# Kernel optimization log

Hardware: AMD Instinct MI355X
Metric: run time of the kernel (lower is better)

The kernel has to match this reference:

```python
import jax, jax.numpy as jnp
import numpy as np

B, N_UNITS, SEQ, H = 4, 1024, 2048, 8
D_HEAD = N_UNITS // H
SCALE = 1.0 / D_HEAD ** 0.5


def setup_inputs() -> dict:
    key = jax.random.key(0)
    k1, k2, k3 = jax.random.split(key, 3)
    x = jax.random.normal(k1, (B, N_UNITS, SEQ), dtype=jnp.float32)
    # conv1x1 weights, bias=False; scaled like typical init
    W_qkv = jax.random.normal(k2, (3 * N_UNITS, N_UNITS), dtype=jnp.float32) * (1.0 / N_UNITS ** 0.5)
    W_out = jax.random.normal(k3, (N_UNITS, N_UNITS), dtype=jnp.float32) * (1.0 / N_UNITS ** 0.5)
    return {"x": x, "W_qkv": W_qkv, "W_out": W_out}


def reference(x, W_qkv, W_out):
    # x: (B, n_units, S). Conv1x1 == per-position linear along channel dim.
    qkv = jnp.einsum('oc,bcs->bos', W_qkv, x)          # (B, 3*n_units, S)
    Q, K, V = jnp.split(qkv, 3, axis=1)                # each (B, n_units, S)
    # torch.chunk along channels into h heads == reshape (B, h, d_head, S)
    Q = Q.reshape(B, H, D_HEAD, SEQ)
    K = K.reshape(B, H, D_HEAD, SEQ)
    V = V.reshape(B, H, D_HEAD, SEQ)
    # scores: Q^T K * scale  (NO softmax in original module; mask unused)
    A = jnp.einsum('bhdq,bhdk->bhqk', Q, K) * SCALE    # (B, h, S, S)
    # aggregation: sum_k A[q,k] * V[d,k]  (original does broadcast mul+sum)
    C = jnp.einsum('bhqk,bhdk->bhdq', A, V)            # (B, h, d_head, S)
    C = C.reshape(B, N_UNITS, SEQ)
    out = jnp.einsum('oc,bcs->bos', W_out, C)          # (B, n_units, S)
    return out
```

## Files before the change

### kernel.cpp

```cpp
#include <hip/hip_runtime.h>
#include <hip/hip_bf16.h>
#include <stdint.h>

using bf16 = __hip_bfloat16;

typedef __bf16 bf16x8 __attribute__((ext_vector_type(8)));
typedef float  f32x4  __attribute__((ext_vector_type(4)));

constexpr int Bc = 4, Hh = 8, Dh = 128, S = 2048, Cn = 1024, O3 = 3072;
constexpr float SCALE = 0.08838834764831845f;

#define GLDS16(gp, lp)                                               \
  __builtin_amdgcn_global_load_lds(                                  \
      (const __attribute__((address_space(1))) void*)(gp),           \
      (__attribute__((address_space(3))) void*)(lp), 16, 0, 0)

#define WAITVM(N) asm volatile("s_waitcnt vmcnt(" #N ")" ::: "memory")
#define BAR()                                  \
  do {                                         \
    asm volatile("" ::: "memory");             \
    __builtin_amdgcn_s_barrier();              \
    asm volatile("" ::: "memory");             \
  } while (0)

__device__ __forceinline__ void gemm_bt_core(
    const bf16* __restrict__ Abase, int lda,
    const bf16* __restrict__ Bbase, int ldb,
    int kIters, f32x4 (&acc)[4][4])
{
  alignas(16) __shared__ bf16 As[128 * 32];
  alignas(16) __shared__ bf16 Bs[128 * 32];
  const int t    = threadIdx.x;
  const int lane = t & 63;
  const int quad = lane >> 4, r16 = lane & 15;
  const int wave = t >> 6;
  const int wm = (wave & 1) * 64, wn = (wave >> 1) * 64;
  const int lrow = lane >> 2;
  const int lk   = (lane & 3) * 8;

  const long aOff0 = (long)(wave * 32 + lrow) * lda + lk;
  const long aOff1 = aOff0 + 16l * lda;
  const long bOff0 = (long)(wave * 32 + lrow) * ldb + lk;
  const long bOff1 = bOff0 + 16l * ldb;
  bf16* aL0 = &As[(wave * 32) * 32];
  bf16* aL1 = &As[(wave * 32 + 16) * 32];
  bf16* bL0 = &Bs[(wave * 32) * 32];
  bf16* bL1 = &Bs[(wave * 32 + 16) * 32];

#pragma unroll
  for (int i = 0; i < 4; i++)
#pragma unroll
    for (int j = 0; j < 4; j++) acc[i][j] = {0.f, 0.f, 0.f, 0.f};

  for (int ks = 0; ks < kIters; ++ks) {
    const int k0 = ks * 32;
    __syncthreads();
    GLDS16(Abase + k0 + aOff0, aL0);
    GLDS16(Abase + k0 + aOff1, aL1);
    GLDS16(Bbase + k0 + bOff0, bL0);
    GLDS16(Bbase + k0 + bOff1, bL1);
    __syncthreads();
    bf16x8 af[4], bfr[4];
#pragma unroll
    for (int i = 0; i < 4; i++)
      af[i] = *(const bf16x8*)&As[(wm + i * 16 + r16) * 32 + quad * 8];
#pragma unroll
    for (int j = 0; j < 4; j++)
      bfr[j] = *(const bf16x8*)&Bs[(wn + j * 16 + r16) * 32 + quad * 8];
#pragma unroll
    for (int i = 0; i < 4; i++)
#pragma unroll
      for (int j = 0; j < 4; j++)
        acc[i][j] = __builtin_amdgcn_mfma_f32_16x16x32_bf16(af[i], bfr[j], acc[i][j], 0, 0, 0);
  }
}

__device__ __forceinline__ void store_bf16_tile(
    f32x4 (&acc)[4][4], bf16* __restrict__ Cp, int ldc)
{
  const int t = threadIdx.x;
  const int lane = t & 63;
  const int quad = lane >> 4, r16 = lane & 15;
  const int wave = t >> 6;
  const int wm = (wave & 1) * 64, wn = (wave >> 1) * 64;
#pragma unroll
  for (int i = 0; i < 4; i++)
#pragma unroll
    for (int j = 0; j < 4; j++)
#pragma unroll
      for (int r = 0; r < 4; r++) {
        const int row = wm + i * 16 + quad * 4 + r;
        const int col = wn + j * 16 + r16;
        Cp[(long)row * ldc + col] = __float2bfloat16(acc[i][j][r]);
      }
}

__device__ __forceinline__ void store_f32_tile(
    f32x4 (&acc)[4][4], float* __restrict__ Cp, int ldc)
{
  const int t = threadIdx.x;
  const int lane = t & 63;
  const int quad = lane >> 4, r16 = lane & 15;
  const int wave = t >> 6;
  const int wm = (wave & 1) * 64, wn = (wave >> 1) * 64;
#pragma unroll
  for (int i = 0; i < 4; i++)
#pragma unroll
    for (int j = 0; j < 4; j++)
#pragma unroll
      for (int r = 0; r < 4; r++) {
        const int row = wm + i * 16 + quad * 4 + r;
        const int col = wn + j * 16 + r16;
        Cp[(long)row * ldc + col] = acc[i][j][r];
      }
}

__global__ __launch_bounds__(512, 2) void k_gemm_kv8(
    const bf16* __restrict__ WkvB, const bf16* __restrict__ xT, bf16* __restrict__ KV)
{
  constexpr int NT = Cn / 32;
  alignas(16) __shared__ bf16 smem[4 * 16384];

  const int orig = blockIdx.x;
  const int swz  = (orig & 7) * 32 + (orig >> 3);
  const int mt = swz >> 5;
  const int nt = swz & 31;
  const int m0 = mt * 256;

  const int tid  = threadIdx.x;
  const int lane = tid & 63;
  const int w    = tid >> 6;
  const int quad = lane >> 4, r16 = lane & 15;
  const int wm = (w >> 2) * 128;
  const int wn = (w & 3) * 64;

  const int srow = w * 16 + (lane >> 2);
  const int cx   = (lane & 3) ^ ((lane >> 3) & 3);
  const bf16* Ag = WkvB + (long)(m0 + srow) * Cn + cx * 8;
  const bf16* Bg = xT + (long)((long)nt * 256 + srow) * Cn + cx * 8;
  const int ldsW = w * 512;

#define KV8_STAGE_A(tt)                                                   \
  do {                                                                    \
    const int k0_ = (tt) * 32, bb_ = ((tt) & 3) * 16384;                  \
    GLDS16(Ag + k0_,            &smem[bb_ + ldsW]);                       \
    GLDS16(Ag + 128l * Cn + k0_, &smem[bb_ + 4096 + ldsW]);               \
  } while (0)
#define KV8_STAGE_B(tt)                                                   \
  do {                                                                    \
    const int k0_ = (tt) * 32, bb_ = ((tt) & 3) * 16384;                  \
    GLDS16(Bg + k0_,            &smem[bb_ + 8192 + ldsW]);                \
    GLDS16(Bg + 128l * Cn + k0_, &smem[bb_ + 8192 + 4096 + ldsW]);        \
  } while (0)

  const int sc8 = (quad ^ ((r16 >> 1) & 3)) * 8;

  f32x4 acc[8][4];
#pragma unroll
  for (int m = 0; m < 8; m++)
#pragma unroll
    for (int n = 0; n < 4; n++) acc[m][n] = {0.f, 0.f, 0.f, 0.f};

  KV8_STAGE_A(0); KV8_STAGE_B(0);
  KV8_STAGE_A(1); KV8_STAGE_B(1);
  KV8_STAGE_A(2); KV8_STAGE_B(2);
  WAITVM(8);
  BAR();

#pragma unroll 2
  for (int tt = 0; tt < NT; ++tt) {
    const bf16* Ab = &smem[(tt & 3) * 16384];
    const bf16* Bb = Ab + 8192;
    bf16x8 af[4], bfr[4];

#pragma unroll
    for (int n = 0; n < 4; n++)
      bfr[n] = *(const bf16x8*)&Bb[(wn + n * 16 + r16) * 32 + sc8];
#pragma unroll
    for (int m = 0; m < 4; m++)
      af[m] = *(const bf16x8*)&Ab[(wm + m * 16 + r16) * 32 + sc8];
    if (tt + 3 < NT) KV8_STAGE_A(tt + 3);
    BAR();
    __builtin_amdgcn_s_setprio(1);
#pragma unroll
    for (int m = 0; m < 4; m++)
#pragma unroll
      for (int n = 0; n < 4; n++)
        acc[m][n] = __builtin_amdgcn_mfma_f32_16x16x32_bf16(af[m], bfr[n], acc[m][n], 0, 0, 0);
    __builtin_amdgcn_s_setprio(0);
    BAR();

#pragma unroll
    for (int m = 0; m < 4; m++)
      af[m] = *(const bf16x8*)&Ab[(wm + (m + 4) * 16 + r16) * 32 + sc8];
    if (tt + 3 < NT) KV8_STAGE_B(tt + 3);
    if (tt <= NT - 4)      { WAITVM(8); }
    else if (tt == NT - 3) { WAITVM(4); }
    else if (tt == NT - 2) { WAITVM(0); }
    BAR();
    __builtin_amdgcn_s_setprio(1);
#pragma unroll
    for (int m = 0; m < 4; m++)
#pragma unroll
      for (int n = 0; n < 4; n++)
        acc[m + 4][n] = __builtin_amdgcn_mfma_f32_16x16x32_bf16(af[m], bfr[n], acc[m + 4][n], 0, 0, 0);
    __builtin_amdgcn_s_setprio(0);
    BAR();
  }

  bf16* Cp = KV + (long)(nt >> 3) * 2048 * S + (long)m0 * S + (nt & 7) * 256;
#pragma unroll
  for (int m = 0; m < 8; m++)
#pragma unroll
    for (int n = 0; n < 4; n++)
#pragma unroll
      for (int r = 0; r < 4; r++) {
        const int row = wm + m * 16 + quad * 4 + r;
        const int col = wn + n * 16 + r16;
        Cp[(long)row * S + col] = __float2bfloat16(acc[m][n][r]);
      }
#undef KV8_STAGE_A
#undef KV8_STAGE_B
}

__global__ __launch_bounds__(256) void k_cvt_w(
    const float* __restrict__ Wkv, const float* __restrict__ Wout,
    bf16* __restrict__ WkvB, bf16* __restrict__ WoutB)
{
  const long v = (long)blockIdx.x * 256 + threadIdx.x;
  const bool isK = v < 524288;
  const float4 f = isK ? ((const float4*)Wkv)[v] : ((const float4*)Wout)[v - 524288];
  bf16 tmp[4];
  tmp[0] = __float2bfloat16(f.x);
  tmp[1] = __float2bfloat16(f.y);
  tmp[2] = __float2bfloat16(f.z);
  tmp[3] = __float2bfloat16(f.w);
  ushort4 u = *(ushort4*)tmp;
  if (isK) ((ushort4*)WkvB)[v] = u;
  else     ((ushort4*)WoutB)[v - 524288] = u;
}

__global__ __launch_bounds__(256) void k_transpose_cvt(
    const float* __restrict__ in, bf16* __restrict__ out, long inZ, long outZ,
    int inld, int outld)
{
  __shared__ bf16 tile[32][33];
  const float* ip = in + (long)blockIdx.z * inZ;
  bf16* op = out + (long)blockIdx.z * outZ;
  const int c0 = blockIdx.x * 32, r0 = blockIdx.y * 32;
  const int tx = threadIdx.x & 31, ty = threadIdx.x >> 5;
#pragma unroll
  for (int i = 0; i < 32; i += 8)
    tile[ty + i][tx] = __float2bfloat16(ip[(long)(r0 + ty + i) * inld + c0 + tx]);
  __syncthreads();
#pragma unroll
  for (int i = 0; i < 32; i += 8)
    op[(long)(c0 + ty + i) * outld + r0 + tx] = tile[tx][ty + i];
}

__global__ __launch_bounds__(256) void k_gemm_mt(
    const bf16* __restrict__ KV, float* __restrict__ MTpart)
{
  const int chunk = blockIdx.x;
  const int z = blockIdx.y;
  const int b = z >> 3, h = z & 7;
  const bf16* base = KV + (long)b * 2048 * S;
  const bf16* A  = base + (long)(h * Dh) * S + chunk * 256;
  const bf16* Bp = base + (long)(1024 + h * Dh) * S + chunk * 256;
  f32x4 acc[4][4];
  gemm_bt_core(A, S, Bp, S, 8, acc);
  store_f32_tile(acc, MTpart + ((long)chunk * 32 + z) * (Dh * Dh), Dh);
}

__global__ __launch_bounds__(256) void k_reduce_mt(
    const float* __restrict__ MTpart, bf16* __restrict__ MbT)
{
  const long i = (long)blockIdx.x * 256 + threadIdx.x;
  float s = 0.f;
#pragma unroll
  for (int c = 0; c < 8; c++) s += MTpart[(long)c * 32 * Dh * Dh + i];
  MbT[i] = __float2bfloat16(s * SCALE);
}

__global__ __launch_bounds__(256) void k_gemm_w2(
    const bf16* __restrict__ WoutB, const bf16* __restrict__ MbT, bf16* __restrict__ W2)
{
  const int m0 = blockIdx.x * 128;
  const int h = blockIdx.y, b = blockIdx.z;
  const int z = b * 8 + h;
  f32x4 acc[4][4];
  gemm_bt_core(WoutB + (long)m0 * Cn + h * Dh, Cn,
               MbT + (long)z * Dh * Dh, Dh, 4, acc);
  store_bf16_tile(acc, W2 + (long)b * Cn * Cn + (long)m0 * Cn + h * Dh, Cn);
}

__global__ __launch_bounds__(256) void k_gemm_w3(
    const bf16* __restrict__ W2, const bf16* __restrict__ WqT, bf16* __restrict__ W3)
{
  const int m0 = blockIdx.x * 128, n0 = blockIdx.y * 128, b = blockIdx.z;
  f32x4 acc[4][4];
  gemm_bt_core(W2 + (long)b * Cn * Cn + (long)m0 * Cn, Cn,
               WqT + (long)n0 * Cn, Cn, Cn / 32, acc);
  store_bf16_tile(acc, W3 + (long)b * Cn * Cn + (long)m0 * Cn + n0, Cn);
}

__global__ __launch_bounds__(256) void k_gemm_out(
    const bf16* __restrict__ W3, const bf16* __restrict__ xT, float* __restrict__ out)
{
  const int m0 = blockIdx.x * 128, n0 = blockIdx.y * 128, b = blockIdx.z;
  f32x4 acc[4][4];
  gemm_bt_core(W3 + (long)b * Cn * Cn + (long)m0 * Cn, Cn,
               xT + (long)b * S * Cn + (long)n0 * Cn, Cn, Cn / 32, acc);
  store_f32_tile(acc, out + (long)b * Cn * S + (long)m0 * S + n0, S);
}

extern "C" void kernel_launch(void* const* d_in, const int* in_sizes, int n_in,
                              void* d_out, int out_size, void* d_ws, size_t ws_size,
                              hipStream_t stream)
{
  const float* x    = (const float*)d_in[0];
  const float* Wqkv = (const float*)d_in[1];
  const float* Wout = (const float*)d_in[2];
  float* out = (float*)d_out;

  char* ws = (char*)d_ws;
  bf16*  KV     = (bf16*)ws;
  bf16*  xT     = (bf16*)(ws + 33554432);
  float* MTpart = (float*)(ws + 50331648);
  bf16*  W3     = (bf16*)(ws + 50331648);
  bf16*  WkvB   = (bf16*)(ws + 67108864);
  bf16*  WoutB  = (bf16*)(ws + 71303168);
  bf16*  WqT    = (bf16*)(ws + 73400320);
  bf16*  MbT    = (bf16*)(ws + 75497472);
  bf16*  W2     = (bf16*)(ws + 76546048);

  k_cvt_w<<<dim3(3072), 256, 0, stream>>>(Wqkv + (long)Cn * Cn, Wout, WkvB, WoutB);
  k_transpose_cvt<<<dim3(64, 32, 4), 256, 0, stream>>>(
      x, xT, (long)1024 * 2048, (long)2048 * 1024, 2048, 1024);
  k_transpose_cvt<<<dim3(32, 32, 1), 256, 0, stream>>>(
      Wqkv, WqT, 0, 0, 1024, 1024);
  k_gemm_kv8<<<dim3(256), 512, 0, stream>>>(WkvB, xT, KV);
  k_gemm_mt<<<dim3(8, 32), 256, 0, stream>>>(KV, MTpart);
  k_reduce_mt<<<dim3(2048), 256, 0, stream>>>(MTpart, MbT);
  k_gemm_w2<<<dim3(8, 8, 4), 256, 0, stream>>>(WoutB, MbT, W2);
  k_gemm_w3<<<dim3(8, 8, 4), 256, 0, stream>>>(W2, WqT, W3);
  k_gemm_out<<<dim3(8, 16, 4), 256, 0, stream>>>(W3, xT, out);
}
```

Baseline: 213.3 us.

## Software-pipeline LDS fragment loads in KV GEMM and add 8-wave output GEMM

The KV projection GEMM main loop is restructured so the next k-step's A/B fragments are read from LDS after the second MFMA half. Both stage loads are issued together at the top, which drops one barrier per iteration. A new 512-thread output GEMM kernel with 128x256 tiles, a 4-stage direct-to-LDS pipeline and a swizzled block order replaces the generic 256-thread output GEMM. The aim is to hide LDS and global latency behind MFMA work, at the cost of more registers and tighter buffer-reuse ordering.

```diff
diff --git a/kernel.cpp b/kernel.cpp
--- a/kernel.cpp
+++ b/kernel.cpp
@@ -143,13 +143,13 @@
 #define KV8_STAGE_A(tt)                                                   \
   do {                                                                    \
     const int k0_ = (tt) * 32, bb_ = ((tt) & 3) * 16384;                  \
-    GLDS16(Ag + k0_,            &smem[bb_ + ldsW]);                       \
+    GLDS16(Ag + k0_,             &smem[bb_ + ldsW]);                      \
     GLDS16(Ag + 128l * Cn + k0_, &smem[bb_ + 4096 + ldsW]);               \
   } while (0)
 #define KV8_STAGE_B(tt)                                                   \
   do {                                                                    \
     const int k0_ = (tt) * 32, bb_ = ((tt) & 3) * 16384;                  \
-    GLDS16(Bg + k0_,            &smem[bb_ + 8192 + ldsW]);                \
+    GLDS16(Bg + k0_,             &smem[bb_ + 8192 + ldsW]);               \
     GLDS16(Bg + 128l * Cn + k0_, &smem[bb_ + 8192 + 4096 + ldsW]);        \
   } while (0)
 
@@ -167,45 +167,58 @@
   WAITVM(8);
   BAR();
 
-#pragma unroll 2
+  bf16x8 af0[4], bfr0[4], af1[4];
+  {
+    const bf16* Ab = &smem[0];
+    const bf16* Bb = Ab + 8192;
+#pragma unroll
+    for (int n = 0; n < 4; n++)
+      bfr0[n] = *(const bf16x8*)&Bb[(wn + n * 16 + r16) * 32 + sc8];
+#pragma unroll
+    for (int m = 0; m < 4; m++)
+      af0[m] = *(const bf16x8*)&Ab[(wm + m * 16 + r16) * 32 + sc8];
+  }
+
+#pragma unroll 4
   for (int tt = 0; tt < NT; ++tt) {
     const bf16* Ab = &smem[(tt & 3) * 16384];
-    const bf16* Bb = Ab + 8192;
-    bf16x8 af[4], bfr[4];
-
-#pragma unroll
-    for (int n = 0; n < 4; n++)
-      bfr[n] = *(const bf16x8*)&Bb[(wn + n * 16 + r16) * 32 + sc8];
+
+    BAR();
+    if (tt + 3 < NT) { KV8_STAGE_A(tt + 3); KV8_STAGE_B(tt + 3); }
 #pragma unroll
     for (int m = 0; m < 4; m++)
-      af[m] = *(const bf16x8*)&Ab[(wm + m * 16 + r16) * 32 + sc8];
-    if (tt + 3 < NT) KV8_STAGE_A(tt + 3);
-    BAR();
+      af1[m] = *(const bf16x8*)&Ab[(wm + (m + 4) * 16 + r16) * 32 + sc8];
     __builtin_amdgcn_s_setprio(1);
 #pragma unroll
     for (int m = 0; m < 4; m++)
 #pragma unroll
       for (int n = 0; n < 4; n++)
-        acc[m][n] = __builtin_amdgcn_mfma_f32_16x16x32_bf16(af[m], bfr[n], acc[m][n], 0, 0, 0);
+        acc[m][n] = __builtin_amdgcn_mfma_f32_16x16x32_bf16(af0[m], bfr0[n], acc[m][n], 0, 0, 0);
     __builtin_amdgcn_s_setprio(0);
-    BAR();
-
-#pragma unroll
-    for (int m = 0; m < 4; m++)
-      af[m] = *(const bf16x8*)&Ab[(wm + (m + 4) * 16 + r16) * 32 + sc8];
-    if (tt + 3 < NT) KV8_STAGE_B(tt + 3);
+
     if (tt <= NT - 4)      { WAITVM(8); }
     else if (tt == NT - 3) { WAITVM(4); }
     else if (tt == NT - 2) { WAITVM(0); }
     BAR();
+
     __builtin_amdgcn_s_setprio(1);
 #pragma unroll
     for (int m = 0; m < 4; m++)
 #pragma unroll
       for (int n = 0; n < 4; n++)
-        acc[m + 4][n] = __builtin_amdgcn_mfma_f32_16x16x32_bf16(af[m], bfr[n], acc[m + 4][n], 0, 0, 0);
+        acc[m + 4][n] = __builtin_amdgcn_mfma_f32_16x16x32_bf16(af1[m], bfr0[n], acc[m + 4][n], 0, 0, 0);
     __builtin_amdgcn_s_setprio(0);
-    BAR();
+
+    if (tt + 1 < NT) {
+      const bf16* Ab2 = &smem[((tt + 1) & 3) * 16384];
+      const bf16* Bb2 = Ab2 + 8192;
+#pragma unroll
+      for (int n = 0; n < 4; n++)
+        bfr0[n] = *(const bf16x8*)&Bb2[(wn + n * 16 + r16) * 32 + sc8];
+#pragma unroll
+      for (int m = 0; m < 4; m++)
+        af0[m] = *(const bf16x8*)&Ab2[(wm + m * 16 + r16) * 32 + sc8];
+    }
   }
 
   bf16* Cp = KV + (long)(nt >> 3) * 2048 * S + (long)m0 * S + (nt & 7) * 256;
@@ -221,6 +234,120 @@
       }
 #undef KV8_STAGE_A
 #undef KV8_STAGE_B
+}
+
+__global__ __launch_bounds__(512, 2) void k_gemm_out8(
+    const bf16* __restrict__ W3, const bf16* __restrict__ xT, float* __restrict__ out)
+{
+  constexpr int NT = Cn / 32;
+  alignas(16) __shared__ bf16 smem[4 * 12288];
+
+  const int orig = blockIdx.x;
+  const int swz  = (orig & 7) * 32 + (orig >> 3);
+  const int b  = swz >> 6;
+  const int mt = (swz >> 3) & 7;
+  const int nt = swz & 7;
+  const int m0 = mt * 128, n0 = nt * 256;
+
+  const int tid  = threadIdx.x;
+  const int lane = tid & 63;
+  const int w    = tid >> 6;
+  const int quad = lane >> 4, r16 = lane & 15;
+  const int wm = (w >> 2) * 64;
+  const int wn = (w & 3) * 64;
+
+  const int srow = w * 16 + (lane >> 2);
+  const int cx   = (lane & 3) ^ ((lane >> 3) & 3);
+  const bf16* Ag = W3 + (long)b * Cn * Cn + (long)(m0 + srow) * Cn + cx * 8;
+  const bf16* Bg = xT + (long)b * S * Cn + (long)(n0 + srow) * Cn + cx * 8;
+  const int ldsW = w * 512;
+
+#define OUT_STAGE(tt)                                                     \
+  do {                                                                    \
+    const int k0_ = (tt) * 32, bb_ = ((tt) & 3) * 12288;                  \
+    GLDS16(Ag + k0_,             &smem[bb_ + ldsW]);                      \
+    GLDS16(Bg + k0_,             &smem[bb_ + 4096 + ldsW]);               \
+    GLDS16(Bg + 128l * Cn + k0_, &smem[bb_ + 8192 + ldsW]);               \
+  } while (0)
+
+  const int sc8 = (quad ^ ((r16 >> 1) & 3)) * 8;
+
+  f32x4 acc[4][4];
+#pragma unroll
+  for (int m = 0; m < 4; m++)
+#pragma unroll
+    for (int n = 0; n < 4; n++) acc[m][n] = {0.f, 0.f, 0.f, 0.f};
+
+  OUT_STAGE(0); OUT_STAGE(1); OUT_STAGE(2);
+  WAITVM(6);
+  BAR();
+
+  bf16x8 af0[2], bfr0[4], af1[2];
+  {
+    const bf16* Ab = &smem[0];
+    const bf16* Bb = Ab + 4096;
+#pragma unroll
+    for (int n = 0; n < 4; n++)
+      bfr0[n] = *(const bf16x8*)&Bb[(wn + n * 16 + r16) * 32 + sc8];
+#pragma unroll
+    for (int m = 0; m < 2; m++)
+      af0[m] = *(const bf16x8*)&Ab[(wm + m * 16 + r16) * 32 + sc8];
+  }
+
+#pragma unroll 4
+  for (int tt = 0; tt < NT; ++tt) {
+    const bf16* Ab = &smem[(tt & 3) * 12288];
+
+    BAR();
+    if (tt + 3 < NT) OUT_STAGE(tt + 3);
+#pragma unroll
+    for (int m = 0; m < 2; m++)
+      af1[m] = *(const bf16x8*)&Ab[(wm + (m + 2) * 16 + r16) * 32 + sc8];
+    __builtin_amdgcn_s_setprio(1);
+#pragma unroll
+    for (int m = 0; m < 2; m++)
+#pragma unroll
+      for (int n = 0; n < 4; n++)
+        acc[m][n] = __builtin_amdgcn_mfma_f32_16x16x32_bf16(af0[m], bfr0[n], acc[m][n], 0, 0, 0);
+    __builtin_amdgcn_s_setprio(0);
+
+    if (tt <= NT - 4)      { WAITVM(6); }
+    else if (tt == NT - 3) { WAITVM(3); }
+    else if (tt == NT - 2) { WAITVM(0); }
+    BAR();
+
+    __builtin_amdgcn_s_setprio(1);
+#pragma unroll
+    for (int m = 0; m < 2; m++)
+#pragma unroll
+      for (int n = 0; n < 4; n++)
+        acc[m + 2][n] = __builtin_amdgcn_mfma_f32_16x16x32_bf16(af1[m], bfr0[n], acc[m + 2][n], 0, 0, 0);
+    __builtin_amdgcn_s_setprio(0);
+
+    if (tt + 1 < NT) {
+      const bf16* Ab2 = &smem[((tt + 1) & 3) * 12288];
+      const bf16* Bb2 = Ab2 + 4096;
+#pragma unroll
+      for (int n = 0; n < 4; n++)
+        bfr0[n] = *(const bf16x8*)&Bb2[(wn + n * 16 + r16) * 32 + sc8];
+#pragma unroll
+      for (int m = 0; m < 2; m++)
+        af0[m] = *(const bf16x8*)&Ab2[(wm + m * 16 + r16) * 32 + sc8];
+    }
+  }
+
+  float* Cp = out + (long)b * Cn * S + (long)m0 * S + n0;
+#pragma unroll
+  for (int m = 0; m < 4; m++)
+#pragma unroll
+    for (int n = 0; n < 4; n++)
+#pragma unroll
+      for (int r = 0; r < 4; r++) {
+        const int row = wm + m * 16 + quad * 4 + r;
+        const int col = wn + n * 16 + r16;
+        Cp[(long)row * S + col] = acc[m][n][r];
+      }
+#undef OUT_STAGE
 }
 
 __global__ __launch_bounds__(256) void k_cvt_w(
@@ -304,16 +431,6 @@
   store_bf16_tile(acc, W3 + (long)b * Cn * Cn + (long)m0 * Cn + n0, Cn);
 }
 
-__global__ __launch_bounds__(256) void k_gemm_out(
-    const bf16* __restrict__ W3, const bf16* __restrict__ xT, float* __restrict__ out)
-{
-  const int m0 = blockIdx.x * 128, n0 = blockIdx.y * 128, b = blockIdx.z;
-  f32x4 acc[4][4];
-  gemm_bt_core(W3 + (long)b * Cn * Cn + (long)m0 * Cn, Cn,
-               xT + (long)b * S * Cn + (long)n0 * Cn, Cn, Cn / 32, acc);
-  store_f32_tile(acc, out + (long)b * Cn * S + (long)m0 * S + n0, S);
-}
-
 extern "C" void kernel_launch(void* const* d_in, const int* in_sizes, int n_in,
                               void* d_out, int out_size, void* d_ws, size_t ws_size,
                               hipStream_t stream)
@@ -344,5 +461,5 @@
   k_reduce_mt<<<dim3(2048), 256, 0, stream>>>(MTpart, MbT);
   k_gemm_w2<<<dim3(8, 8, 4), 256, 0, stream>>>(WoutB, MbT, W2);
   k_gemm_w3<<<dim3(8, 8, 4), 256, 0, stream>>>(W2, WqT, W3);
-  k_gemm_out<<<dim3(8, 16, 4), 256, 0, stream>>>(W3, xT, out);
-}
+  k_gemm_out8<<<dim3(256), 512, 0, stream>>>(W3, xT, out);
+}
```

Measured after the change: 202.9 us. 4.9% less time.
